# Optimization experiments

Hardware: AMD Instinct MI355X
Metric: run time of the kernel (lower is better)

Reference implementation:

```python
import jax, jax.numpy as jnp
import numpy as np

E = 1024      # hidden_size
H = 16        # num_attention_heads
HD = E // H   # head_dim
EPS = 1e-5


def _mw_linear(x, Wt, bt, Wi, bi, split):
    # multiway linear: text weights on tokens [:split], image weights on [split:]
    xt = x[:, :split] @ Wt.T + bt
    xi = x[:, split:] @ Wi.T + bi
    return jnp.concatenate([xt, xi], axis=1)


def _ln(x, g, b):
    mu = jnp.mean(x, axis=-1, keepdims=True)
    var = jnp.mean(jnp.square(x - mu), axis=-1, keepdims=True)
    return (x - mu) * jax.lax.rsqrt(var + EPS) * g + b


def _mw_ln(x, gt, bt, gi, bi, split):
    return jnp.concatenate([_ln(x[:, :split], gt, bt), _ln(x[:, split:], gi, bi)], axis=1)


def setup_inputs() -> dict:
    key = jax.random.key(0)
    ks = jax.random.split(key, 24)
    B, T = 8, 1024
    d = {
        'query': jax.random.normal(ks[0], (B, T, E), jnp.float32),
        'key': jax.random.normal(ks[1], (B, T, E), jnp.float32),
        'value': jax.random.normal(ks[2], (B, T, E), jnp.float32),
        'attention_mask': jax.random.normal(ks[3], (T, T), jnp.float32) * 0.02,
    }
    i = 4
    for name in ['q', 'k', 'v', 'o']:
        d[f'W{name}_t'] = jax.random.normal(ks[i], (E, E), jnp.float32) * 0.02; i += 1
        d[f'b{name}_t'] = jnp.zeros((E,), jnp.float32)
        d[f'W{name}_i'] = jax.random.normal(ks[i], (E, E), jnp.float32) * 0.02; i += 1
        d[f'b{name}_i'] = jnp.zeros((E,), jnp.float32)
    d['ln_g_t'] = jnp.ones((E,), jnp.float32)
    d['ln_b_t'] = jnp.zeros((E,), jnp.float32)
    d['ln_g_i'] = jnp.ones((E,), jnp.float32)
    d['ln_b_i'] = jnp.zeros((E,), jnp.float32)
    d['split_position'] = 64
    return d


def reference(query, key, value, attention_mask,
              Wq_t, bq_t, Wq_i, bq_i,
              Wk_t, bk_t, Wk_i, bk_i,
              Wv_t, bv_t, Wv_i, bv_i,
              Wo_t, bo_t, Wo_i, bo_i,
              ln_g_t, ln_b_t, ln_g_i, ln_b_i,
              split_position):
    B, T, _ = query.shape
    S = key.shape[1]
    scaling = HD ** -0.5
    q = _mw_linear(query, Wq_t, bq_t, Wq_i, bq_i, split_position) * scaling
    k = _mw_linear(key, Wk_t, bk_t, Wk_i, bk_i, split_position)
    v = _mw_linear(value, Wv_t, bv_t, Wv_i, bv_i, split_position)
    q = q.reshape(B, T, H, HD)
    k = k.reshape(B, S, H, HD)
    v = v.reshape(B, S, H, HD)
    # [B, H, T, S] attention logits
    attn_weights = jnp.einsum('bthd,bshd->bhts', q, k)
    attn_weights = jnp.nan_to_num(attn_weights) + attention_mask[None, None]
    probs = jax.nn.softmax(attn_weights.astype(jnp.float32), axis=-1).astype(attn_weights.dtype)
    attn = jnp.einsum('bhts,bshd->bthd', probs, v).reshape(B, T, E)
    attn = _mw_ln(attn, ln_g_t, ln_b_t, ln_g_i, ln_b_i, split_position)
    attn = _mw_linear(attn, Wo_t, bo_t, Wo_i, bo_i, split_position)
    return attn
```

## Files before the change

### kernel.cpp

```cpp
#include <hip/hip_runtime.h>

#define E_DIM 1024
#define HEADS 16
#define HD 64

typedef unsigned short ushort_t;
typedef __attribute__((ext_vector_type(8))) short bf16x8;
typedef __attribute__((ext_vector_type(4))) float floatx4;

__device__ inline unsigned int pack2bf(float a, float b) {
    unsigned int ua = __builtin_bit_cast(unsigned int, a);
    unsigned int ub = __builtin_bit_cast(unsigned int, b);
    ua = (ua + 0x8000u) >> 16;
    ub = (ub + 0x8000u) & 0xFFFF0000u;
    return ua | ub;
}
__device__ inline unsigned short f2bf(float a) {
    return (unsigned short)((__builtin_bit_cast(unsigned int, a) + 0x8000u) >> 16);
}
__device__ inline float bf2f(unsigned int s) {
    return __builtin_bit_cast(float, s << 16);
}

__device__ __forceinline__ void load_lds16(const void* g, void* l) {
    __builtin_amdgcn_global_load_lds(
        (const __attribute__((address_space(1))) unsigned int*)g,
        (__attribute__((address_space(3))) unsigned int*)l, 16, 0, 0);
}

__global__ __launch_bounds__(256) void cvt_inputs(
    const float* s0, const float* s1, const float* s2,
    ushort_t* d0, ushort_t* d1, ushort_t* d2)
{
    const float* __restrict__ src = (blockIdx.y == 0) ? s0 : (blockIdx.y == 1) ? s1 : s2;
    ushort_t* __restrict__ dst = (blockIdx.y == 0) ? d0 : (blockIdx.y == 1) ? d1 : d2;
    size_t i = ((size_t)blockIdx.x * 256 + threadIdx.x) * 8;
    float4 a = *(const float4*)&src[i];
    float4 b = *(const float4*)&src[i + 4];
    uint4 o;
    o.x = pack2bf(a.x, a.y); o.y = pack2bf(a.z, a.w);
    o.z = pack2bf(b.x, b.y); o.w = pack2bf(b.z, b.w);
    *(uint4*)&dst[i] = o;
}

__global__ __launch_bounds__(256) void cvt_weights(
    const float* w0, const float* w1, const float* w2, const float* w3,
    const float* w4, const float* w5, const float* w6, const float* w7,
    ushort_t* __restrict__ out)
{
    const float* srcs[8] = {w0, w1, w2, w3, w4, w5, w6, w7};
    const float* __restrict__ src = srcs[blockIdx.y];
    ushort_t* __restrict__ dst = out + (size_t)blockIdx.y * E_DIM * E_DIM;
    size_t i = ((size_t)blockIdx.x * 256 + threadIdx.x) * 8;
    float4 a = *(const float4*)&src[i];
    float4 b = *(const float4*)&src[i + 4];
    uint4 o;
    o.x = pack2bf(a.x, a.y); o.y = pack2bf(a.z, a.w);
    o.z = pack2bf(b.x, b.y); o.w = pack2bf(b.z, b.w);
    *(uint4*)&dst[i] = o;
}

template<bool OUT_BF16>
__device__ __forceinline__ void gemm_core(
    const ushort_t* __restrict__ x, const ushort_t* __restrict__ W,
    const float* __restrict__ bias, void* __restrict__ outv,
    int m0, int n0, int split, int kind, float scale, int T_)
{
    __shared__ __align__(16) ushort_t As[128 * 32];
    __shared__ __align__(16) ushort_t Bs[128 * 32];

    const int tid  = threadIdx.x;
    const int lane = tid & 63;
    const int wv   = tid >> 6;
    const int rw   = (wv >> 1) * 64;
    const int cw   = (wv & 1) * 64;
    const int am   = lane & 15;
    const int aq   = lane >> 4;

    const int grow = wv * 32 + (lane >> 2);
    const int gcol = (lane & 3) * 8;

    floatx4 acc[4][4];
    #pragma unroll
    for (int i = 0; i < 4; ++i)
        #pragma unroll
        for (int j = 0; j < 4; ++j)
            acc[i][j] = (floatx4){0.f, 0.f, 0.f, 0.f};

    for (int k0 = 0; k0 < E_DIM; k0 += 32) {
        load_lds16(&x[(size_t)(m0 + grow) * E_DIM + k0 + gcol],      &As[(wv * 32) * 32]);
        load_lds16(&x[(size_t)(m0 + grow + 16) * E_DIM + k0 + gcol], &As[(wv * 32 + 16) * 32]);
        load_lds16(&W[(size_t)(n0 + grow) * E_DIM + k0 + gcol],      &Bs[(wv * 32) * 32]);
        load_lds16(&W[(size_t)(n0 + grow + 16) * E_DIM + k0 + gcol], &Bs[(wv * 32 + 16) * 32]);
        __syncthreads();

        bf16x8 af[4], bfv[4];
        #pragma unroll
        for (int i = 0; i < 4; ++i)
            af[i] = *(const bf16x8*)&As[(rw + i * 16 + am) * 32 + aq * 8];
        #pragma unroll
        for (int j = 0; j < 4; ++j)
            bfv[j] = *(const bf16x8*)&Bs[(cw + j * 16 + am) * 32 + aq * 8];

        #pragma unroll
        for (int i = 0; i < 4; ++i)
            #pragma unroll
            for (int j = 0; j < 4; ++j)
                acc[i][j] = __builtin_amdgcn_mfma_f32_16x16x32_bf16(af[i], bfv[j], acc[i][j], 0, 0, 0);
        __syncthreads();
    }

    const int cq = lane >> 4;
    const int cm = lane & 15;
    #pragma unroll
    for (int j = 0; j < 4; ++j) {
        int n = n0 + cw + j * 16 + cm;
        float bv = bias[n];
        #pragma unroll
        for (int i = 0; i < 4; ++i) {
            int mbase = m0 + rw + i * 16 + cq * 4;
            #pragma unroll
            for (int r = 0; r < 4; ++r) {
                int m = mbase + r;
                int t = m % T_;
                if (((t < split) ? 0 : 1) != kind) continue;
                float val = (acc[i][j][r] + bv) * scale;
                if (OUT_BF16) ((ushort_t*)outv)[(size_t)m * E_DIM + n] = f2bf(val);
                else          ((float*)outv)[(size_t)m * E_DIM + n] = val;
            }
        }
    }
}

__global__ __launch_bounds__(256) void gemm_qkv(
    const ushort_t* __restrict__ xq, const ushort_t* __restrict__ xk,
    const ushort_t* __restrict__ xv, const ushort_t* __restrict__ wall,
    const float* bq_t, const float* bq_i, const float* bk_t, const float* bk_i,
    const float* bv_t, const float* bv_i,
    ushort_t* oq, ushort_t* ok, ushort_t* ov,
    const int* __restrict__ split_ptr, int T_)
{
    const int split = *split_ptr;
    const int z = blockIdx.z;
    const int op = z >> 1;
    const int kind = z & 1;
    const int m0 = blockIdx.y * 128;
    const int n0 = blockIdx.x * 128;
    const int t0 = m0 % T_;

    if (kind == 0) { if (t0 >= split) return; }
    else           { if (t0 + 128 <= split) return; }

    const ushort_t* x = (op == 0) ? xq : (op == 1) ? xk : xv;
    ushort_t* outp    = (op == 0) ? oq : (op == 1) ? ok : ov;
    const ushort_t* W = wall + (size_t)z * E_DIM * E_DIM;
    const float* bias = (op == 0) ? (kind ? bq_i : bq_t)
                      : (op == 1) ? (kind ? bk_i : bk_t)
                                  : (kind ? bv_i : bv_t);
    float scale = (op == 0) ? 0.125f : 1.0f;

    gemm_core<true>(x, W, bias, outp, m0, n0, split, kind, scale, T_);
}

__global__ __launch_bounds__(256) void gemm_o(
    const ushort_t* __restrict__ x, const ushort_t* __restrict__ Wt,
    const float* bt, const ushort_t* __restrict__ Wi, const float* bi,
    float* __restrict__ outp, const int* __restrict__ split_ptr, int T_)
{
    const int split = *split_ptr;
    const int kind = blockIdx.z;
    const int m0 = blockIdx.y * 128;
    const int n0 = blockIdx.x * 128;
    const int t0 = m0 % T_;

    if (kind == 0) { if (t0 >= split) return; }
    else           { if (t0 + 128 <= split) return; }

    gemm_core<false>(x, kind ? Wi : Wt, kind ? bi : bt, outp, m0, n0, split, kind, 1.0f, T_);
}

__global__ __launch_bounds__(256) void attn_mfma2(
    const ushort_t* __restrict__ q, const ushort_t* __restrict__ k,
    const ushort_t* __restrict__ v, const float* __restrict__ mask,
    ushort_t* __restrict__ outp, int T_)
{
    const int tid  = threadIdx.x;
    const int lane = tid & 63;
    const int wv   = tid >> 6;
    const int h    = blockIdx.y;
    const int b    = blockIdx.z;
    const int r0   = blockIdx.x * 128;

    __shared__ __align__(16) unsigned short Qs[2 * 128 * 40];
    __shared__ __align__(16) unsigned short Ks[2 * 64 * 40];
    __shared__ __align__(16) unsigned short Vst[2 * 64 * 40];
    __shared__ __align__(16) unsigned short Ps[4 * 2 * 16 * 40];

    const int m    = lane & 15;
    const int kq   = lane >> 4;
    const int wrow = wv * 16;

    #pragma unroll
    for (int i = 0; i < 8; ++i) {
        int f   = tid + 256 * i;
        int row = f >> 4;
        int c4  = (f & 15) * 4;
        uint2 a2 = *(const uint2*)&q[((size_t)(b * T_ + r0 + row)) * E_DIM + h * HD + c4];
        int ad = (c4 >> 5) * 5120 + row * 40 + (c4 & 31);
        *(unsigned int*)&Qs[ad]     = a2.x;
        *(unsigned int*)&Qs[ad + 2] = a2.y;
    }
    __syncthreads();

    bf16x8 aq[2][2];
    #pragma unroll
    for (int qs = 0; qs < 2; ++qs)
        #pragma unroll
        for (int c = 0; c < 2; ++c)
            aq[qs][c] = *(const bf16x8*)&Qs[c * 5120 + (qs * 64 + wrow + m) * 40 + kq * 8];

    floatx4 oa[2][4];
    float mrun[2][4], lsum[2][4];
    #pragma unroll
    for (int qs = 0; qs < 2; ++qs)
        #pragma unroll
        for (int j = 0; j < 4; ++j) {
            oa[qs][j] = (floatx4){0.f, 0.f, 0.f, 0.f};
            mrun[qs][j] = -3.0e38f; lsum[qs][j] = 0.f;
        }

    const int vs0 = (tid >> 4) * 4;
    const int vd0 = (tid & 15) * 4;

    #pragma unroll 1
    for (int s0 = 0; s0 < T_; s0 += 64) {
        __syncthreads();

        #pragma unroll
        for (int i = 0; i < 4; ++i) {
            int f   = tid + 256 * i;
            int row = f >> 4;
            int c4  = (f & 15) * 4;
            uint2 a2 = *(const uint2*)&k[((size_t)(b * T_ + s0 + row)) * E_DIM + h * HD + c4];
            int ad = (c4 >> 5) * 2560 + row * 40 + (c4 & 31);
            *(unsigned int*)&Ks[ad]     = a2.x;
            *(unsigned int*)&Ks[ad + 2] = a2.y;
        }

        {
            uint2 vvr[4];
            #pragma unroll
            for (int i = 0; i < 4; ++i)
                vvr[i] = *(const uint2*)&v[((size_t)(b * T_ + s0 + vs0 + i)) * E_DIM + h * HD + vd0];
            const ushort_t* vp = (const ushort_t*)vvr;
            int plane = (vs0 >> 5) * 2560;
            int sin   = vs0 & 31;
            #pragma unroll
            for (int t = 0; t < 4; ++t) {
                int d  = vd0 + t;
                int pr = d ^ ((d >> 4) & 3);
                uint2 w;
                w.x = (unsigned int)vp[0 * 4 + t] | ((unsigned int)vp[1 * 4 + t] << 16);
                w.y = (unsigned int)vp[2 * 4 + t] | ((unsigned int)vp[3 * 4 + t] << 16);
                *(uint2*)&Vst[plane + pr * 40 + sin] = w;
            }
        }

        __syncthreads();

        #pragma unroll
        for (int qs = 0; qs < 2; ++qs) {
            float mv[4][4];
            {
                const float* mbase = &mask[(size_t)(r0 + qs * 64 + wrow + kq * 4) * T_ + s0 + m];
                #pragma unroll
                for (int j = 0; j < 4; ++j)
                    #pragma unroll
                    for (int r = 0; r < 4; ++r)
                        mv[j][r] = mbase[r * T_ + j * 16];
            }

            floatx4 sa[4];
            #pragma unroll
            for (int j = 0; j < 4; ++j) sa[j] = (floatx4){0.f, 0.f, 0.f, 0.f};
            #pragma unroll
            for (int c = 0; c < 2; ++c) {
                #pragma unroll
                for (int j = 0; j < 4; ++j) {
                    bf16x8 bk = *(const bf16x8*)&Ks[c * 2560 + (j * 16 + m) * 40 + kq * 8];
                    sa[j] = __builtin_amdgcn_mfma_f32_16x16x32_bf16(aq[qs][c], bk, sa[j], 0, 0, 0);
                }
            }

            float mnew[4], alpha[4];
            #pragma unroll
            for (int r = 0; r < 4; ++r) {
                sa[0][r] += mv[0][r]; sa[1][r] += mv[1][r];
                sa[2][r] += mv[2][r]; sa[3][r] += mv[3][r];
                float mt = fmaxf(fmaxf(sa[0][r], sa[1][r]), fmaxf(sa[2][r], sa[3][r]));
                mt = fmaxf(mt, __shfl_xor(mt, 1));
                mt = fmaxf(mt, __shfl_xor(mt, 2));
                mt = fmaxf(mt, __shfl_xor(mt, 4));
                mt = fmaxf(mt, __shfl_xor(mt, 8));
                float mn = fmaxf(mrun[qs][r], mt);
                alpha[r] = __expf(mrun[qs][r] - mn);
                mnew[r] = mn;
                mrun[qs][r] = mn;
            }
            #pragma unroll
            for (int j = 0; j < 4; ++j)
                #pragma unroll
                for (int r = 0; r < 4; ++r)
                    oa[qs][j][r] *= alpha[r];

            float rs[4] = {0.f, 0.f, 0.f, 0.f};
            #pragma unroll
            for (int j = 0; j < 4; ++j) {
                int gl = ((((j & 1) << 1) | (m >> 3)) ^ kq) & 3;
                int pbase = wv * 1280 + (j >> 1) * 640 + (kq * 4) * 40 + gl * 8 + (m & 7);
                #pragma unroll
                for (int r = 0; r < 4; ++r) {
                    float p = __expf(sa[j][r] - mnew[r]);
                    rs[r] += p;
                    Ps[pbase + r * 40] = f2bf(p);
                }
            }
            #pragma unroll
            for (int r = 0; r < 4; ++r) {
                float s = rs[r];
                s += __shfl_xor(s, 1); s += __shfl_xor(s, 2);
                s += __shfl_xor(s, 4); s += __shfl_xor(s, 8);
                lsum[qs][r] = lsum[qs][r] * alpha[r] + s;
            }

            #pragma unroll
            for (int c = 0; c < 2; ++c) {
                bf16x8 ap = *(const bf16x8*)&Ps[wv * 1280 + c * 640 + m * 40 + ((kq ^ (m >> 2)) & 3) * 8];
                #pragma unroll
                for (int j = 0; j < 4; ++j) {
                    int pr = 16 * j + (m ^ j);
                    bf16x8 bv = *(const bf16x8*)&Vst[c * 2560 + pr * 40 + kq * 8];
                    oa[qs][j] = __builtin_amdgcn_mfma_f32_16x16x32_bf16(ap, bv, oa[qs][j], 0, 0, 0);
                }
            }
        }
    }

    #pragma unroll
    for (int qs = 0; qs < 2; ++qs)
        #pragma unroll
        for (int r = 0; r < 4; ++r) {
            float inv = 1.0f / lsum[qs][r];
            size_t orow = ((size_t)(b * T_ + r0 + qs * 64 + wrow + kq * 4 + r)) * E_DIM + h * HD;
            #pragma unroll
            for (int j = 0; j < 4; ++j)
                outp[orow + j * 16 + m] = f2bf(oa[qs][j][r] * inv);
        }
}

__global__ __launch_bounds__(256) void mw_ln_bf16(
    const ushort_t* __restrict__ x,
    const float* __restrict__ gt, const float* __restrict__ bt,
    const float* __restrict__ gi, const float* __restrict__ bi,
    ushort_t* __restrict__ out,
    const int* __restrict__ split_ptr, int T_)
{
    const int split = *split_ptr;
    const int row = blockIdx.x;
    const int t = row % T_;
    const float* __restrict__ g  = (t < split) ? gt : gi;
    const float* __restrict__ bb = (t < split) ? bt : bi;

    const int tid = threadIdx.x;
    const int lane = tid & 63;
    const int wid = tid >> 6;

    __shared__ float red[8];

    uint2 xv = *(const uint2*)&x[(size_t)row * E_DIM + tid * 4];
    float f0 = bf2f(xv.x & 0xffffu), f1 = bf2f(xv.x >> 16);
    float f2 = bf2f(xv.y & 0xffffu), f3 = bf2f(xv.y >> 16);
    float s = f0 + f1 + f2 + f3;
    #pragma unroll
    for (int off = 1; off < 64; off <<= 1) s += __shfl_xor(s, off, 64);
    if (lane == 0) red[wid] = s;
    __syncthreads();
    float mu = (red[0] + red[1] + red[2] + red[3]) * (1.0f / E_DIM);

    float d0 = f0 - mu, d1 = f1 - mu, d2 = f2 - mu, d3 = f3 - mu;
    float s2 = d0*d0 + d1*d1 + d2*d2 + d3*d3;
    #pragma unroll
    for (int off = 1; off < 64; off <<= 1) s2 += __shfl_xor(s2, off, 64);
    if (lane == 0) red[4 + wid] = s2;
    __syncthreads();
    float var = (red[4] + red[5] + red[6] + red[7]) * (1.0f / E_DIM);
    float rstd = rsqrtf(var + 1e-5f);

    float4 gv = *(const float4*)&g[tid * 4];
    float4 bv = *(const float4*)&bb[tid * 4];
    uint2 ov;
    ov.x = pack2bf(d0 * rstd * gv.x + bv.x, d1 * rstd * gv.y + bv.y);
    ov.y = pack2bf(d2 * rstd * gv.z + bv.z, d3 * rstd * gv.w + bv.w);
    *(uint2*)&out[(size_t)row * E_DIM + tid * 4] = ov;
}

extern "C" void kernel_launch(void* const* d_in, const int* in_sizes, int n_in,
                              void* d_out, int out_size, void* d_ws, size_t ws_size,
                              hipStream_t stream) {
    const float* query = (const float*)d_in[0];
    const float* key   = (const float*)d_in[1];
    const float* value = (const float*)d_in[2];
    const float* mask  = (const float*)d_in[3];
    const float* Wq_t = (const float*)d_in[4];  const float* bq_t = (const float*)d_in[5];
    const float* Wq_i = (const float*)d_in[6];  const float* bq_i = (const float*)d_in[7];
    const float* Wk_t = (const float*)d_in[8];  const float* bk_t = (const float*)d_in[9];
    const float* Wk_i = (const float*)d_in[10]; const float* bk_i = (const float*)d_in[11];
    const float* Wv_t = (const float*)d_in[12]; const float* bv_t = (const float*)d_in[13];
    const float* Wv_i = (const float*)d_in[14]; const float* bv_i = (const float*)d_in[15];
    const float* Wo_t = (const float*)d_in[16]; const float* bo_t = (const float*)d_in[17];
    const float* Wo_i = (const float*)d_in[18]; const float* bo_i = (const float*)d_in[19];
    const float* ln_g_t = (const float*)d_in[20]; const float* ln_b_t = (const float*)d_in[21];
    const float* ln_g_i = (const float*)d_in[22]; const float* ln_b_i = (const float*)d_in[23];
    const int* split = (const int*)d_in[24];

    float* out = (float*)d_out;

    const int BT = in_sizes[0] / E_DIM;
    const int T_ = 1024;
    const int B  = BT / T_;

    ushort_t* ws = (ushort_t*)d_ws;
    const size_t nx = (size_t)BT * E_DIM;
    const size_t nw = (size_t)E_DIM * E_DIM;
    ushort_t* xq_bf = ws;
    ushort_t* xk_bf = ws + nx;
    ushort_t* xv_bf = ws + 2 * nx;
    ushort_t* k_bf  = ws + 3 * nx;
    ushort_t* v_bf  = ws + 4 * nx;
    ushort_t* w_bf  = ws + 5 * nx;
    ushort_t* q_bf  = (ushort_t*)d_out;

    dim3 blk(256);
    const int cvt_blocks = (int)(nx / 2048);
    const int wcvt_blocks = (int)(nw / 2048);

    cvt_weights<<<dim3(wcvt_blocks, 8), blk, 0, stream>>>(
        Wq_t, Wq_i, Wk_t, Wk_i, Wv_t, Wv_i, Wo_t, Wo_i, w_bf);
    cvt_inputs<<<dim3(cvt_blocks, 3), blk, 0, stream>>>(
        query, key, value, xq_bf, xk_bf, xv_bf);

    gemm_qkv<<<dim3(E_DIM / 128, BT / 128, 6), blk, 0, stream>>>(
        xq_bf, xk_bf, xv_bf, w_bf,
        bq_t, bq_i, bk_t, bk_i, bv_t, bv_i,
        q_bf, k_bf, v_bf, split, T_);

    attn_mfma2<<<dim3(T_ / 128, HEADS, B), blk, 0, stream>>>(
        q_bf, k_bf, v_bf, mask, q_bf, T_);

    mw_ln_bf16<<<dim3(BT), blk, 0, stream>>>(
        q_bf, ln_g_t, ln_b_t, ln_g_i, ln_b_i, xq_bf, split, T_);

    gemm_o<<<dim3(E_DIM / 128, BT / 128, 2), blk, 0, stream>>>(
        xq_bf, w_bf + 6 * nw, bo_t, w_bf + 7 * nw, bo_i, out, split, T_);
}
```

Measured before the change: 503.2 us.

## Double GEMM K-tile with XOR-swizzled LDS; load attention Q fragments directly from global

The shared GEMM core now stages a K-slice of 64 instead of 32 per iteration. The As/Bs tiles use an XOR swizzle so the 16-byte fragment reads avoid LDS bank conflicts, and this halves the number of barrier pairs per GEMM. The attention kernel drops the Q staging buffer in LDS and its extra barrier, reading each wave's Q MFMA fragments straight from global memory. In exchange the GEMM uses twice the LDS per block, which can cut occupancy, and the Q loads become less coalesced.

```diff
diff --git a/kernel.cpp b/kernel.cpp
--- a/kernel.cpp
+++ b/kernel.cpp
@@ -66,8 +66,8 @@
     const float* __restrict__ bias, void* __restrict__ outv,
     int m0, int n0, int split, int kind, float scale, int T_)
 {
-    __shared__ __align__(16) ushort_t As[128 * 32];
-    __shared__ __align__(16) ushort_t Bs[128 * 32];
+    __shared__ __align__(16) ushort_t As[128 * 64];
+    __shared__ __align__(16) ushort_t Bs[128 * 64];
 
     const int tid  = threadIdx.x;
     const int lane = tid & 63;
@@ -77,8 +77,8 @@
     const int am   = lane & 15;
     const int aq   = lane >> 4;
 
-    const int grow = wv * 32 + (lane >> 2);
-    const int gcol = (lane & 3) * 8;
+    const int srow = lane >> 3;
+    const int sg   = ((lane & 7) ^ (srow & 7)) * 8;
 
     floatx4 acc[4][4];
     #pragma unroll
@@ -87,26 +87,34 @@
         for (int j = 0; j < 4; ++j)
             acc[i][j] = (floatx4){0.f, 0.f, 0.f, 0.f};
 
-    for (int k0 = 0; k0 < E_DIM; k0 += 32) {
-        load_lds16(&x[(size_t)(m0 + grow) * E_DIM + k0 + gcol],      &As[(wv * 32) * 32]);
-        load_lds16(&x[(size_t)(m0 + grow + 16) * E_DIM + k0 + gcol], &As[(wv * 32 + 16) * 32]);
-        load_lds16(&W[(size_t)(n0 + grow) * E_DIM + k0 + gcol],      &Bs[(wv * 32) * 32]);
-        load_lds16(&W[(size_t)(n0 + grow + 16) * E_DIM + k0 + gcol], &Bs[(wv * 32 + 16) * 32]);
+    for (int k0 = 0; k0 < E_DIM; k0 += 64) {
+        #pragma unroll
+        for (int i = 0; i < 4; ++i) {
+            int r = wv * 32 + i * 8;
+            load_lds16(&x[(size_t)(m0 + r + srow) * E_DIM + k0 + sg], &As[r * 64]);
+            load_lds16(&W[(size_t)(n0 + r + srow) * E_DIM + k0 + sg], &Bs[r * 64]);
+        }
         __syncthreads();
 
-        bf16x8 af[4], bfv[4];
-        #pragma unroll
-        for (int i = 0; i < 4; ++i)
-            af[i] = *(const bf16x8*)&As[(rw + i * 16 + am) * 32 + aq * 8];
-        #pragma unroll
-        for (int j = 0; j < 4; ++j)
-            bfv[j] = *(const bf16x8*)&Bs[(cw + j * 16 + am) * 32 + aq * 8];
-
-        #pragma unroll
-        for (int i = 0; i < 4; ++i)
-            #pragma unroll
-            for (int j = 0; j < 4; ++j)
-                acc[i][j] = __builtin_amdgcn_mfma_f32_16x16x32_bf16(af[i], bfv[j], acc[i][j], 0, 0, 0);
+        #pragma unroll
+        for (int kk = 0; kk < 64; kk += 32) {
+            bf16x8 af[4], bfv[4];
+            #pragma unroll
+            for (int i = 0; i < 4; ++i) {
+                int row = rw + i * 16 + am;
+                af[i] = *(const bf16x8*)&As[row * 64 + ((((kk >> 3) + aq) ^ (row & 7)) << 3)];
+            }
+            #pragma unroll
+            for (int j = 0; j < 4; ++j) {
+                int row = cw + j * 16 + am;
+                bfv[j] = *(const bf16x8*)&Bs[row * 64 + ((((kk >> 3) + aq) ^ (row & 7)) << 3)];
+            }
+            #pragma unroll
+            for (int i = 0; i < 4; ++i)
+                #pragma unroll
+                for (int j = 0; j < 4; ++j)
+                    acc[i][j] = __builtin_amdgcn_mfma_f32_16x16x32_bf16(af[i], bfv[j], acc[i][j], 0, 0, 0);
+        }
         __syncthreads();
     }
 
@@ -179,7 +187,7 @@
     gemm_core<false>(x, kind ? Wi : Wt, kind ? bi : bt, outp, m0, n0, split, kind, 1.0f, T_);
 }
 
-__global__ __launch_bounds__(256) void attn_mfma2(
+__global__ __launch_bounds__(256) void attn_mfma3(
     const ushort_t* __restrict__ q, const ushort_t* __restrict__ k,
     const ushort_t* __restrict__ v, const float* __restrict__ mask,
     ushort_t* __restrict__ outp, int T_)
@@ -191,7 +199,6 @@
     const int b    = blockIdx.z;
     const int r0   = blockIdx.x * 128;
 
-    __shared__ __align__(16) unsigned short Qs[2 * 128 * 40];
     __shared__ __align__(16) unsigned short Ks[2 * 64 * 40];
     __shared__ __align__(16) unsigned short Vst[2 * 64 * 40];
     __shared__ __align__(16) unsigned short Ps[4 * 2 * 16 * 40];
@@ -200,24 +207,13 @@
     const int kq   = lane >> 4;
     const int wrow = wv * 16;
 
-    #pragma unroll
-    for (int i = 0; i < 8; ++i) {
-        int f   = tid + 256 * i;
-        int row = f >> 4;
-        int c4  = (f & 15) * 4;
-        uint2 a2 = *(const uint2*)&q[((size_t)(b * T_ + r0 + row)) * E_DIM + h * HD + c4];
-        int ad = (c4 >> 5) * 5120 + row * 40 + (c4 & 31);
-        *(unsigned int*)&Qs[ad]     = a2.x;
-        *(unsigned int*)&Qs[ad + 2] = a2.y;
-    }
-    __syncthreads();
-
     bf16x8 aq[2][2];
     #pragma unroll
     for (int qs = 0; qs < 2; ++qs)
         #pragma unroll
         for (int c = 0; c < 2; ++c)
-            aq[qs][c] = *(const bf16x8*)&Qs[c * 5120 + (qs * 64 + wrow + m) * 40 + kq * 8];
+            aq[qs][c] = *(const bf16x8*)&q[((size_t)(b * T_ + r0 + qs * 64 + wrow + m)) * E_DIM
+                                           + h * HD + c * 32 + kq * 8];
 
     floatx4 oa[2][4];
     float mrun[2][4], lsum[2][4];
@@ -454,7 +450,7 @@
         bq_t, bq_i, bk_t, bk_i, bv_t, bv_i,
         q_bf, k_bf, v_bf, split, T_);
 
-    attn_mfma2<<<dim3(T_ / 128, HEADS, B), blk, 0, stream>>>(
+    attn_mfma3<<<dim3(T_ / 128, HEADS, B), blk, 0, stream>>>(
         q_bf, k_bf, v_bf, mask, q_bf, T_);
 
     mw_ln_bf16<<<dim3(BT), blk, 0, stream>>>(
```

Result: slower. 536.0 us (+6.5%).

## Double-buffer K/V tiles in attention with register prefetch, load Q directly

Applied to the files above, without the earlier changes.

Attention now loads the next K/V tile into registers while computing on the current tile and writes it to a second LDS buffer afterwards, so each iteration needs one barrier instead of two. The Q staging through LDS is removed and Q fragments are read straight from global memory. This hides global load latency behind MFMA work and softmax, at the cost of extra registers and doubled K/V LDS. Because the attention output overwrites q_bf in place, the direct Q reads could race with other blocks' output writes, but those rows are separate per block, so it stays safe.

```diff
diff --git a/kernel.cpp b/kernel.cpp
--- a/kernel.cpp
+++ b/kernel.cpp
@@ -179,7 +179,7 @@
     gemm_core<false>(x, kind ? Wi : Wt, kind ? bi : bt, outp, m0, n0, split, kind, 1.0f, T_);
 }
 
-__global__ __launch_bounds__(256) void attn_mfma2(
+__global__ __launch_bounds__(256) void attn_mfma4(
     const ushort_t* __restrict__ q, const ushort_t* __restrict__ k,
     const ushort_t* __restrict__ v, const float* __restrict__ mask,
     ushort_t* __restrict__ outp, int T_)
@@ -191,33 +191,21 @@
     const int b    = blockIdx.z;
     const int r0   = blockIdx.x * 128;
 
-    __shared__ __align__(16) unsigned short Qs[2 * 128 * 40];
-    __shared__ __align__(16) unsigned short Ks[2 * 64 * 40];
-    __shared__ __align__(16) unsigned short Vst[2 * 64 * 40];
-    __shared__ __align__(16) unsigned short Ps[4 * 2 * 16 * 40];
+    __shared__ __align__(16) unsigned short Ks[2 * 5120];
+    __shared__ __align__(16) unsigned short Vst[2 * 5120];
+    __shared__ __align__(16) unsigned short Ps[4 * 1280];
 
     const int m    = lane & 15;
     const int kq   = lane >> 4;
     const int wrow = wv * 16;
 
-    #pragma unroll
-    for (int i = 0; i < 8; ++i) {
-        int f   = tid + 256 * i;
-        int row = f >> 4;
-        int c4  = (f & 15) * 4;
-        uint2 a2 = *(const uint2*)&q[((size_t)(b * T_ + r0 + row)) * E_DIM + h * HD + c4];
-        int ad = (c4 >> 5) * 5120 + row * 40 + (c4 & 31);
-        *(unsigned int*)&Qs[ad]     = a2.x;
-        *(unsigned int*)&Qs[ad + 2] = a2.y;
-    }
-    __syncthreads();
-
     bf16x8 aq[2][2];
     #pragma unroll
     for (int qs = 0; qs < 2; ++qs)
         #pragma unroll
         for (int c = 0; c < 2; ++c)
-            aq[qs][c] = *(const bf16x8*)&Qs[c * 5120 + (qs * 64 + wrow + m) * 40 + kq * 8];
+            aq[qs][c] = *(const bf16x8*)&q[((size_t)(b * T_ + r0 + qs * 64 + wrow + m)) * E_DIM
+                                           + h * HD + c * 32 + kq * 8];
 
     floatx4 oa[2][4];
     float mrun[2][4], lsum[2][4];
@@ -229,44 +217,59 @@
             mrun[qs][j] = -3.0e38f; lsum[qs][j] = 0.f;
         }
 
-    const int vs0 = (tid >> 4) * 4;
-    const int vd0 = (tid & 15) * 4;
-
+    const int krow = tid >> 4;
+    const int kc4  = (tid & 15) * 4;
+    const int kad  = (kc4 >> 5) * 2560 + krow * 40 + (kc4 & 31);
+    const int vs0  = (tid >> 4) * 4;
+    const int vd0  = (tid & 15) * 4;
+    const int vplane = (vs0 >> 5) * 2560;
+    const int vsin   = vs0 & 31;
+
+    uint2 kreg[4], vreg[4];
+
+    #pragma unroll
+    for (int i = 0; i < 4; ++i)
+        kreg[i] = *(const uint2*)&k[((size_t)(b * T_ + krow + 16 * i)) * E_DIM + h * HD + kc4];
+    #pragma unroll
+    for (int i = 0; i < 4; ++i)
+        vreg[i] = *(const uint2*)&v[((size_t)(b * T_ + vs0 + i)) * E_DIM + h * HD + vd0];
+
+    #pragma unroll
+    for (int i = 0; i < 4; ++i) {
+        int ad = kad + 16 * i * 40;
+        *(unsigned int*)&Ks[ad]     = kreg[i].x;
+        *(unsigned int*)&Ks[ad + 2] = kreg[i].y;
+    }
+    {
+        const ushort_t* vp = (const ushort_t*)vreg;
+        #pragma unroll
+        for (int t = 0; t < 4; ++t) {
+            int d  = vd0 + t;
+            int pr = d ^ ((d >> 4) & 3);
+            uint2 w;
+            w.x = (unsigned int)vp[0 * 4 + t] | ((unsigned int)vp[1 * 4 + t] << 16);
+            w.y = (unsigned int)vp[2 * 4 + t] | ((unsigned int)vp[3 * 4 + t] << 16);
+            *(uint2*)&Vst[vplane + pr * 40 + vsin] = w;
+        }
+    }
+    __syncthreads();
+
+    const int NT = T_ / 64;
     #pragma unroll 1
-    for (int s0 = 0; s0 < T_; s0 += 64) {
-        __syncthreads();
-
-        #pragma unroll
-        for (int i = 0; i < 4; ++i) {
-            int f   = tid + 256 * i;
-            int row = f >> 4;
-            int c4  = (f & 15) * 4;
-            uint2 a2 = *(const uint2*)&k[((size_t)(b * T_ + s0 + row)) * E_DIM + h * HD + c4];
-            int ad = (c4 >> 5) * 2560 + row * 40 + (c4 & 31);
-            *(unsigned int*)&Ks[ad]     = a2.x;
-            *(unsigned int*)&Ks[ad + 2] = a2.y;
-        }
-
-        {
-            uint2 vvr[4];
+    for (int it = 0; it < NT; ++it) {
+        const int cur = (it & 1) * 5120;
+        const int nxt = ((it + 1) & 1) * 5120;
+        const int s0 = it * 64;
+
+        if (it + 1 < NT) {
+            int s0n = s0 + 64;
             #pragma unroll
             for (int i = 0; i < 4; ++i)
-                vvr[i] = *(const uint2*)&v[((size_t)(b * T_ + s0 + vs0 + i)) * E_DIM + h * HD + vd0];
-            const ushort_t* vp = (const ushort_t*)vvr;
-            int plane = (vs0 >> 5) * 2560;
-            int sin   = vs0 & 31;
-            #pragma unroll
-            for (int t = 0; t < 4; ++t) {
-                int d  = vd0 + t;
-                int pr = d ^ ((d >> 4) & 3);
-                uint2 w;
-                w.x = (unsigned int)vp[0 * 4 + t] | ((unsigned int)vp[1 * 4 + t] << 16);
-                w.y = (unsigned int)vp[2 * 4 + t] | ((unsigned int)vp[3 * 4 + t] << 16);
-                *(uint2*)&Vst[plane + pr * 40 + sin] = w;
-            }
-        }
-
-        __syncthreads();
+                kreg[i] = *(const uint2*)&k[((size_t)(b * T_ + s0n + krow + 16 * i)) * E_DIM + h * HD + kc4];
+            #pragma unroll
+            for (int i = 0; i < 4; ++i)
+                vreg[i] = *(const uint2*)&v[((size_t)(b * T_ + s0n + vs0 + i)) * E_DIM + h * HD + vd0];
+        }
 
         #pragma unroll
         for (int qs = 0; qs < 2; ++qs) {
@@ -287,7 +290,7 @@
             for (int c = 0; c < 2; ++c) {
                 #pragma unroll
                 for (int j = 0; j < 4; ++j) {
-                    bf16x8 bk = *(const bf16x8*)&Ks[c * 2560 + (j * 16 + m) * 40 + kq * 8];
+                    bf16x8 bk = *(const bf16x8*)&Ks[cur + c * 2560 + (j * 16 + m) * 40 + kq * 8];
                     sa[j] = __builtin_amdgcn_mfma_f32_16x16x32_bf16(aq[qs][c], bk, sa[j], 0, 0, 0);
                 }
             }
@@ -339,10 +342,30 @@
                 #pragma unroll
                 for (int j = 0; j < 4; ++j) {
                     int pr = 16 * j + (m ^ j);
-                    bf16x8 bv = *(const bf16x8*)&Vst[c * 2560 + pr * 40 + kq * 8];
+                    bf16x8 bv = *(const bf16x8*)&Vst[cur + c * 2560 + pr * 40 + kq * 8];
                     oa[qs][j] = __builtin_amdgcn_mfma_f32_16x16x32_bf16(ap, bv, oa[qs][j], 0, 0, 0);
                 }
             }
+        }
+
+        if (it + 1 < NT) {
+            #pragma unroll
+            for (int i = 0; i < 4; ++i) {
+                int ad = nxt + kad + 16 * i * 40;
+                *(unsigned int*)&Ks[ad]     = kreg[i].x;
+                *(unsigned int*)&Ks[ad + 2] = kreg[i].y;
+            }
+            const ushort_t* vp = (const ushort_t*)vreg;
+            #pragma unroll
+            for (int t = 0; t < 4; ++t) {
+                int d  = vd0 + t;
+                int pr = d ^ ((d >> 4) & 3);
+                uint2 w;
+                w.x = (unsigned int)vp[0 * 4 + t] | ((unsigned int)vp[1 * 4 + t] << 16);
+                w.y = (unsigned int)vp[2 * 4 + t] | ((unsigned int)vp[3 * 4 + t] << 16);
+                *(uint2*)&Vst[nxt + vplane + pr * 40 + vsin] = w;
+            }
+            __syncthreads();
         }
     }
 
@@ -454,7 +477,7 @@
         bq_t, bq_i, bk_t, bk_i, bv_t, bv_i,
         q_bf, k_bf, v_bf, split, T_);
 
-    attn_mfma2<<<dim3(T_ / 128, HEADS, B), blk, 0, stream>>>(
+    attn_mfma4<<<dim3(T_ / 128, HEADS, B), blk, 0, stream>>>(
         q_bf, k_bf, v_bf, mask, q_bf, T_);
 
     mw_ln_bf16<<<dim3(BT), blk, 0, stream>>>(
```

Measured after the change: 499.1 us. About the same (-0.8%).
